# Performance work log

Measured on AMD Instinct MI355X. Metric: run time of the kernel, lower is better.

## Reference

```python
import jax, jax.numpy as jnp
import numpy as np

NUM_HEADS = 16
ROPE_BASE = 10000.0
NEG_INF = float('-inf')


def _rotate_half_interleaved(x):
    # x: [..., d]; interleaved rotation: (-x2, x1) pairs
    x1 = x[..., ::2]
    x2 = x[..., 1::2]
    return jnp.stack((-x2, x1), axis=-1).reshape(x.shape)


def _rope_tables(seq_len, head_dim, dtype):
    inv_freq = 1.0 / (ROPE_BASE ** (jnp.arange(0, head_dim, 2, dtype=jnp.float32) / head_dim))
    pos = jnp.arange(seq_len, dtype=jnp.float32)
    freqs = pos[:, None] * inv_freq[None, :]          # [S, d/2]
    emb = jnp.concatenate((freqs, freqs), axis=-1)    # [S, d]  (HF-style concat, as in source)
    return jnp.cos(emb).astype(dtype), jnp.sin(emb).astype(dtype)


def setup_inputs() -> dict:
    key = jax.random.key(0)
    ks = jax.random.split(key, 4)
    B, S, H = 2, 2048, 2048
    scale = 0.02
    x = jax.random.normal(ks[0], (B, S, H), dtype=jnp.float32)
    qkv_w = jax.random.normal(ks[1], (3 * H, H), dtype=jnp.float32) * scale
    qkv_b = jnp.zeros((3 * H,), dtype=jnp.float32)
    out_w = jax.random.normal(ks[2], (H, H), dtype=jnp.float32) * scale
    out_b = jnp.zeros((H,), dtype=jnp.float32)
    attention_mask = jnp.ones((B, S), dtype=jnp.int32)
    return {"x": x, "attention_mask": attention_mask, "qkv_w": qkv_w,
            "qkv_b": qkv_b, "out_w": out_w, "out_b": out_b}


def reference(x, attention_mask, qkv_w, qkv_b, out_w, out_b):
    B, S, H = x.shape
    nh = NUM_HEADS
    hd = H // nh
    scale = hd ** -0.5

    qkv = x @ qkv_w.T + qkv_b                            # [B,S,3H]
    qkv = qkv.reshape(B, S, 3, nh, hd).transpose(2, 0, 3, 1, 4)  # [3,B,nh,S,hd]
    q, k, v = qkv[0], qkv[1], qkv[2]

    cos, sin = _rope_tables(S, hd, x.dtype)              # [S,hd]
    cos = cos[None, None, :, :]
    sin = sin[None, None, :, :]
    q = q * cos + _rotate_half_interleaved(q) * sin
    k = k * cos + _rotate_half_interleaved(k) * sin

    scores = jnp.einsum('bhqd,bhkd->bhqk', q, k) * scale  # [B,nh,S,S]
    causal = jnp.triu(jnp.ones((S, S), dtype=bool), k=1)
    scores = jnp.where(causal[None, None], NEG_INF, scores)
    key_mask = (attention_mask == 0)[:, None, None, :]    # [B,1,1,S]
    scores = jnp.where(key_mask, NEG_INF, scores)

    weights = jax.nn.softmax(scores, axis=-1)
    attn = jnp.einsum('bhqk,bhkd->bhqd', weights, v)       # [B,nh,S,hd]
    attn = attn.transpose(0, 2, 1, 3).reshape(B, S, H)
    return attn @ out_w.T + out_b
```

## Files before the change

### kernel.cpp

```cpp
#include <hip/hip_runtime.h>

typedef __bf16 bf16;
typedef __bf16 bf16x2 __attribute__((ext_vector_type(2)));
typedef __bf16 bf16x4 __attribute__((ext_vector_type(4)));
typedef __bf16 bf16x8 __attribute__((ext_vector_type(8)));
typedef float f32x4 __attribute__((ext_vector_type(4)));
typedef float f32x16 __attribute__((ext_vector_type(16)));

#define MFMA_BF16(a, b, c) __builtin_amdgcn_mfma_f32_16x16x32_bf16(a, b, c, 0, 0, 0)
#define MFMA32(a, b, c)    __builtin_amdgcn_mfma_f32_32x32x16_bf16(a, b, c, 0, 0, 0)

__device__ __forceinline__ void async16(const void* g, void* l) {
    __builtin_amdgcn_global_load_lds(
        (const __attribute__((address_space(1))) void*)g,
        (__attribute__((address_space(3))) void*)l,
        16, 0, 0);
}

__device__ __forceinline__ unsigned pack2(float a, float b) {
    bf16x2 t; t[0] = (bf16)a; t[1] = (bf16)b;
    return __builtin_bit_cast(unsigned, t);
}

__global__ void cvt8(const float* __restrict__ in, bf16* __restrict__ out, int n) {
    int i = (blockIdx.x * 256 + threadIdx.x) * 8;
    if (i >= n) return;
    float4 a = *(const float4*)(in + i);
    float4 b = *(const float4*)(in + i + 4);
    bf16x8 o;
    o[0] = (bf16)a.x; o[1] = (bf16)a.y; o[2] = (bf16)a.z; o[3] = (bf16)a.w;
    o[4] = (bf16)b.x; o[5] = (bf16)b.y; o[6] = (bf16)b.z; o[7] = (bf16)b.w;
    *(bf16x8*)(out + i) = o;
}

__global__ void tables_k(const int* __restrict__ am, float* __restrict__ cosT,
                         float* __restrict__ sinT, float* __restrict__ mbias) {
    int i = blockIdx.x * 256 + threadIdx.x;
    int s = i >> 7, d = i & 127, fi = d & 63;
    float inv = exp2f(-(float)fi * (13.287712379549449f / 64.0f));
    float ang = (float)s * inv;
    cosT[i] = cosf(ang);
    sinT[i] = sinf(ang);
    if (i < 2 * 2048) mbias[i] = (am[i] == 0) ? -1.4427e30f : 0.0f;
}

template <int EPI>
__global__ void __launch_bounds__(256, 2)
gemm_bt(const bf16* __restrict__ A, const bf16* __restrict__ Bt,
        const float* __restrict__ bias, float* __restrict__ Cf,
        bf16* __restrict__ qb, bf16* __restrict__ kb, bf16* __restrict__ vtb,
        const float* __restrict__ cosT, const float* __restrict__ sinT,
        int M, int N, int K, int bn0) {
    __shared__ __align__(16) bf16 sA[128 * 64];
    __shared__ __align__(16) bf16 sB[128 * 64];
    const int tid  = threadIdx.x;
    const int lane = tid & 63;
    const int quad = lane >> 4, l15 = lane & 15;
    const int wid = tid >> 6, wm = wid >> 1, wn = wid & 1;
    const int bm = blockIdx.x, bn = blockIdx.y + bn0;

    f32x4 acc[4][4];
#pragma unroll
    for (int i = 0; i < 4; i++)
#pragma unroll
        for (int j = 0; j < 4; j++)
#pragma unroll
            for (int c = 0; c < 4; c++) acc[i][j][c] = 0.0f;

    const int r0 = tid >> 3, x0 = tid & 7;
    const int g0 = x0 ^ (r0 & 7);
    const bf16* pa = A  + (size_t)(bm * 128 + r0) * K + g0 * 8;
    const bf16* pb = Bt + (size_t)(bn * 128 + r0) * K + g0 * 8;
    bf16* la = sA + tid * 8;
    bf16* lb = sB + tid * 8;
    const size_t gstep = (size_t)32 * K;

    for (int k0 = 0; k0 < K; k0 += 64) {
#pragma unroll
        for (int i = 0; i < 4; i++) {
            async16(pa + i * gstep, la + i * 2048);
            async16(pb + i * gstep, lb + i * 2048);
        }
        pa += 64; pb += 64;
        __syncthreads();
#pragma unroll
        for (int ks = 0; ks < 2; ks++) {
            bf16x8 af[4], bfr[4];
#pragma unroll
            for (int i = 0; i < 4; i++) {
                int r = wm * 64 + i * 16 + l15;
                int x = (ks * 4 + quad) ^ (r & 7);
                af[i] = *(const bf16x8*)(sA + r * 64 + x * 8);
            }
#pragma unroll
            for (int i = 0; i < 4; i++) {
                int r = wn * 64 + i * 16 + l15;
                int x = (ks * 4 + quad) ^ (r & 7);
                bfr[i] = *(const bf16x8*)(sB + r * 64 + x * 8);
            }
#pragma unroll
            for (int mi = 0; mi < 4; mi++)
#pragma unroll
                for (int ni = 0; ni < 4; ni++)
                    acc[mi][ni] = MFMA_BF16(af[mi], bfr[ni], acc[mi][ni]);
        }
        __syncthreads();
    }

    if (EPI == 0) {
#pragma unroll
        for (int mi = 0; mi < 4; mi++)
#pragma unroll
            for (int ni = 0; ni < 4; ni++) {
                int row0 = bm * 128 + wm * 64 + mi * 16 + quad * 4;
                int col  = bn * 128 + wn * 64 + ni * 16 + l15;
                float bv = bias[col];
#pragma unroll
                for (int r = 0; r < 4; r++)
                    Cf[(size_t)(row0 + r) * N + col] = acc[mi][ni][r] + bv;
            }
    } else {
#pragma unroll
        for (int mi = 0; mi < 4; mi++)
#pragma unroll
            for (int ni = 0; ni < 4; ni++) {
                int col   = bn * 128 + wn * 64 + ni * 16 + l15;
                int which = col >> 11;
                int hcol  = col & 2047;
                int h = hcol >> 7, d = hcol & 127;
                float bv = bias[col];
#pragma unroll
                for (int r = 0; r < 4; r++) {
                    int row = bm * 128 + wm * 64 + mi * 16 + quad * 4 + r;
                    int b = row >> 11, s = row & 2047;
                    float v  = acc[mi][ni][r] + bv;
                    float vp = __shfl_xor(v, 1, 64);
                    float ov = v;
                    if (which < 2) {
                        float c  = cosT[(s << 7) + d];
                        float sn = sinT[(s << 7) + d];
                        ov = v * c + ((d & 1) ? vp : -vp) * sn;
                    }
                    if (which == 0) ov *= 0.12751743f;
                    size_t bh = (size_t)(b * 16 + h);
                    if (which == 0)      qb[(bh * 2048 + s) * 128 + d] = (bf16)ov;
                    else if (which == 1) kb[(bh * 2048 + s) * 128 + d] = (bf16)ov;
                    else                 vtb[(bh * 128 + d) * 2048 + s] = (bf16)ov;
                }
            }
    }
}

__global__ void __launch_bounds__(256, 2)
fattn(const bf16* __restrict__ Q, const bf16* __restrict__ Kg,
      const bf16* __restrict__ Vt, const float* __restrict__ mbias,
      bf16* __restrict__ O) {
    __shared__ __align__(16) bf16 sK[2][64 * 128];
    __shared__ __align__(16) bf16 sV[2][128 * 64];
    const int tid = threadIdx.x, lane = tid & 63, w = tid >> 6;
    const int l31 = lane & 31, half = lane >> 5;
    const int id = (int)blockIdx.x;
    const int round = id >> 8, u = id & 255;
    const int bh = u & 31, j8 = u >> 5;
    const int qt = round ? j8 : 15 - j8;
    const int b = bh >> 4, hh = bh & 15;
    const int myq = qt * 128 + w * 32 + l31;
    const int qmin = qt * 128 + w * 32;

    const bf16* Qb  = Q  + (size_t)bh * 2048 * 128;
    const bf16* Kbh = Kg + (size_t)bh * 2048 * 128;
    const bf16* Vbh = Vt + (size_t)bh * 128 * 2048;
    const float* mbb = mbias + b * 2048;

    const int swk = (l31 & 15) ^ (l31 >> 4);
    const int swv = (l31 & 7) ^ ((l31 >> 3) & 3);

    bf16x8 qf[8];
#pragma unroll
    for (int kq = 0; kq < 8; kq++)
        qf[kq] = *(const bf16x8*)(Qb + (size_t)myq * 128 + kq * 16 + half * 8);

    f32x16 oacc[4];
#pragma unroll
    for (int dt = 0; dt < 4; dt++)
#pragma unroll
        for (int c = 0; c < 16; c++) oacc[dt][c] = 0.0f;
    float m_s = -3e38f, l_s = 0.0f;

    const int rk = tid >> 4, xk = tid & 15, gkb = xk ^ rk;
    const int rv = tid >> 3, xv = tid & 7;
    const int gv = xv ^ (rv & 7) ^ ((rv >> 3) & 3);
    const int nkt = 2 * qt + 2;

#pragma unroll
    for (int i = 0; i < 4; i++) {
        async16(Kbh + (size_t)(rk + i * 16) * 128 + (gkb ^ (i & 1)) * 8,
                &sK[0][(i * 256 + tid) * 8]);
        async16(Vbh + (size_t)(rv + i * 32) * 2048 + gv * 8,
                &sV[0][(i * 256 + tid) * 8]);
    }
    __syncthreads();

    for (int kt = 0; kt < nkt; kt++) {
        const int kb0 = kt * 64;
        const int buf = kt & 1;
        if (kt + 1 < nkt) {
            const int nb0 = kb0 + 64;
#pragma unroll
            for (int i = 0; i < 4; i++) {
                async16(Kbh + (size_t)(nb0 + rk + i * 16) * 128 + (gkb ^ (i & 1)) * 8,
                        &sK[buf ^ 1][(i * 256 + tid) * 8]);
                async16(Vbh + (size_t)(rv + i * 32) * 2048 + nb0 + gv * 8,
                        &sV[buf ^ 1][(i * 256 + tid) * 8]);
            }
        }
        const bf16* sKb = sK[buf];
        const bf16* sVb = sV[buf];

        f32x16 sacc[2];
#pragma unroll
        for (int t = 0; t < 2; t++)
#pragma unroll
            for (int c = 0; c < 16; c++) sacc[t][c] = 0.0f;
#pragma unroll
        for (int kq = 0; kq < 8; kq++) {
#pragma unroll
            for (int t = 0; t < 2; t++) {
                int row = t * 32 + l31;
                int x = (kq * 2 + half) ^ swk;
                bf16x8 kf = *(const bf16x8*)(sKb + row * 128 + x * 8);
                sacc[t] = MFMA32(kf, qf[kq], sacc[t]);
            }
        }

        float mx = -3e38f;
        if (kb0 + 63 < qmin) {
#pragma unroll
            for (int t = 0; t < 2; t++)
#pragma unroll
                for (int g = 0; g < 4; g++) {
                    float4 mb4 = *(const float4*)(mbb + kb0 + t * 32 + 8 * g + 4 * half);
#pragma unroll
                    for (int r2 = 0; r2 < 4; r2++) {
                        float v = sacc[t][g * 4 + r2] + ((const float*)&mb4)[r2];
                        sacc[t][g * 4 + r2] = v;
                        mx = fmaxf(mx, v);
                    }
                }
        } else {
#pragma unroll
            for (int t = 0; t < 2; t++)
#pragma unroll
                for (int g = 0; g < 4; g++) {
                    float4 mb4 = *(const float4*)(mbb + kb0 + t * 32 + 8 * g + 4 * half);
#pragma unroll
                    for (int r2 = 0; r2 < 4; r2++) {
                        int sk = kb0 + t * 32 + 8 * g + 4 * half + r2;
                        float v = sacc[t][g * 4 + r2] + ((const float*)&mb4)[r2];
                        v = (sk > myq) ? -1e30f : v;
                        sacc[t][g * 4 + r2] = v;
                        mx = fmaxf(mx, v);
                    }
                }
        }

        mx = fmaxf(mx, __shfl_xor(mx, 32, 64));
        float mnew  = fmaxf(m_s, mx);
        float alpha = exp2f(m_s - mnew);
        float rs = 0.0f;
#pragma unroll
        for (int t = 0; t < 2; t++)
#pragma unroll
            for (int c = 0; c < 16; c++) {
                float p = exp2f(sacc[t][c] - mnew);
                sacc[t][c] = p;
                rs += p;
            }
        l_s = l_s * alpha + rs;
        m_s = mnew;
#pragma unroll
        for (int dt = 0; dt < 4; dt++) oacc[dt] *= alpha;

#pragma unroll
        for (int t = 0; t < 2; t++) {
            unsigned w8[8];
#pragma unroll
            for (int i = 0; i < 8; i++)
                w8[i] = pack2(sacc[t][2 * i], sacc[t][2 * i + 1]);
#pragma unroll
            for (int s2 = 0; s2 < 2; s2++) {
                const int bse = 4 * s2;
                unsigned a0 = half ? w8[bse]     : w8[bse + 2];
                unsigned a1 = half ? w8[bse + 1] : w8[bse + 3];
                unsigned z0 = (unsigned)__shfl_xor((int)a0, 32, 64);
                unsigned z1 = (unsigned)__shfl_xor((int)a1, 32, 64);
                union { unsigned u[4]; bf16x8 v; } pu;
                pu.u[0] = half ? z0 : w8[bse];
                pu.u[1] = half ? z1 : w8[bse + 1];
                pu.u[2] = half ? w8[bse + 2] : z0;
                pu.u[3] = half ? w8[bse + 3] : z1;
                bf16x8 pf = pu.v;
                const int c = (t * 2 + s2) * 2 + half;
#pragma unroll
                for (int dt = 0; dt < 4; dt++) {
                    int row = dt * 32 + l31;
                    int x = c ^ swv;
                    bf16x8 vf = *(const bf16x8*)(sVb + row * 64 + x * 8);
                    oacc[dt] = MFMA32(vf, pf, oacc[dt]);
                }
            }
        }
        __syncthreads();
    }

    l_s += __shfl_xor(l_s, 32, 64);
    float inv = 1.0f / l_s;
    size_t base = ((size_t)(b * 2048 + myq)) * 2048 + hh * 128;
#pragma unroll
    for (int dt = 0; dt < 4; dt++)
#pragma unroll
        for (int g = 0; g < 4; g++) {
            bf16x4 o4;
#pragma unroll
            for (int r2 = 0; r2 < 4; r2++) o4[r2] = (bf16)(oacc[dt][g * 4 + r2] * inv);
            *(bf16x4*)(O + base + dt * 32 + 8 * g + 4 * half) = o4;
        }
}

extern "C" void kernel_launch(void* const* d_in, const int* in_sizes, int n_in,
                              void* d_out, int out_size, void* d_ws, size_t ws_size,
                              hipStream_t stream) {
    const float* x     = (const float*)d_in[0];
    const int*   am    = (const int*)d_in[1];
    const float* qkvw  = (const float*)d_in[2];
    const float* qkvb  = (const float*)d_in[3];
    const float* outw  = (const float*)d_in[4];
    const float* outb  = (const float*)d_in[5];
    float* out = (float*)d_out;

    char* ws = (char*)d_ws;
    bf16*  xb    = (bf16*)(ws);
    bf16*  wqkv  = (bf16*)(ws + (16ull << 20));
    bf16*  wout  = (bf16*)(ws + (40ull << 20));
    bf16*  qb    = (bf16*)(ws + (48ull << 20));
    bf16*  kb    = (bf16*)(ws + (64ull << 20));
    bf16*  vtb   = (bf16*)(ws + (80ull << 20));
    bf16*  attn  = (bf16*)(ws + (96ull << 20));
    float* cosT  = (float*)(ws + (112ull << 20));
    float* sinT  = (float*)(ws + (113ull << 20));
    float* mbias = (float*)(ws + (114ull << 20));

    cvt8<<<4096, 256, 0, stream>>>(x, xb, 4096 * 2048);
    cvt8<<<6144, 256, 0, stream>>>(qkvw, wqkv, 6144 * 2048);
    cvt8<<<2048, 256, 0, stream>>>(outw, wout, 2048 * 2048);
    tables_k<<<1024, 256, 0, stream>>>(am, cosT, sinT, mbias);

    gemm_bt<1><<<dim3(32, 24), 256, 0, stream>>>(
        xb, wqkv, qkvb, nullptr, qb, kb, vtb, cosT, sinT, 4096, 6144, 2048, 0);
    gemm_bt<1><<<dim3(32, 24), 256, 0, stream>>>(
        xb, wqkv, qkvb, nullptr, qb, kb, vtb, cosT, sinT, 4096, 6144, 2048, 24);

    fattn<<<dim3(512), 256, 0, stream>>>(qb, kb, vtb, mbias, attn);

    gemm_bt<0><<<dim3(32, 16), 256, 0, stream>>>(
        attn, wout, outb, out, nullptr, nullptr, nullptr, nullptr, nullptr,
        4096, 2048, 2048, 0);
}
```

Measured before the change: 409.9 us.

## Balance causal attention work with split-KV pairing and fuse prep kernels

The attention kernel now gives every block exactly 17 key tiles. One role computes the first 17 KV tiles of a long query tile and writes fp32 partials. The other role finishes that long tile's remaining tiles, writes a second partial, then processes a short query tile completely. A new combine kernel merges the two partials with log-sum-exp weights. The four conversion/table kernels are fused into one launch and the QKV GEMM is launched once instead of twice, trading extra partial-buffer traffic and a combine pass for even load across blocks and fewer launches.

```diff
diff --git a/kernel.cpp b/kernel.cpp
--- a/kernel.cpp
+++ b/kernel.cpp
@@ -22,9 +22,9 @@
     return __builtin_bit_cast(unsigned, t);
 }
 
-__global__ void cvt8(const float* __restrict__ in, bf16* __restrict__ out, int n) {
-    int i = (blockIdx.x * 256 + threadIdx.x) * 8;
-    if (i >= n) return;
+__device__ __forceinline__ void cvt8_body(const float* __restrict__ in,
+                                          bf16* __restrict__ out, int blk) {
+    int i = (blk * 256 + (int)threadIdx.x) * 8;
     float4 a = *(const float4*)(in + i);
     float4 b = *(const float4*)(in + i + 4);
     bf16x8 o;
@@ -33,15 +33,24 @@
     *(bf16x8*)(out + i) = o;
 }
 
-__global__ void tables_k(const int* __restrict__ am, float* __restrict__ cosT,
-                         float* __restrict__ sinT, float* __restrict__ mbias) {
-    int i = blockIdx.x * 256 + threadIdx.x;
-    int s = i >> 7, d = i & 127, fi = d & 63;
-    float inv = exp2f(-(float)fi * (13.287712379549449f / 64.0f));
-    float ang = (float)s * inv;
-    cosT[i] = cosf(ang);
-    sinT[i] = sinf(ang);
-    if (i < 2 * 2048) mbias[i] = (am[i] == 0) ? -1.4427e30f : 0.0f;
+__global__ void prep(const float* __restrict__ x, const float* __restrict__ qkvw,
+                     const float* __restrict__ outw, const int* __restrict__ am,
+                     bf16* __restrict__ xb, bf16* __restrict__ wqkv, bf16* __restrict__ wout,
+                     float* __restrict__ cosT, float* __restrict__ sinT,
+                     float* __restrict__ mbias) {
+    int blk = blockIdx.x;
+    if (blk < 4096)        cvt8_body(x,    xb,   blk);
+    else if (blk < 10240)  cvt8_body(qkvw, wqkv, blk - 4096);
+    else if (blk < 12288)  cvt8_body(outw, wout, blk - 10240);
+    else {
+        int i = (blk - 12288) * 256 + threadIdx.x;
+        int s = i >> 7, d = i & 127, fi = d & 63;
+        float inv = exp2f(-(float)fi * (13.287712379549449f / 64.0f));
+        float ang = (float)s * inv;
+        cosT[i] = cosf(ang);
+        sinT[i] = sinf(ang);
+        if (i < 2 * 2048) mbias[i] = (am[i] == 0) ? -1.4427e30f : 0.0f;
+    }
 }
 
 template <int EPI>
@@ -50,14 +59,14 @@
         const float* __restrict__ bias, float* __restrict__ Cf,
         bf16* __restrict__ qb, bf16* __restrict__ kb, bf16* __restrict__ vtb,
         const float* __restrict__ cosT, const float* __restrict__ sinT,
-        int M, int N, int K, int bn0) {
+        int M, int N, int K) {
     __shared__ __align__(16) bf16 sA[128 * 64];
     __shared__ __align__(16) bf16 sB[128 * 64];
     const int tid  = threadIdx.x;
     const int lane = tid & 63;
     const int quad = lane >> 4, l15 = lane & 15;
     const int wid = tid >> 6, wm = wid >> 1, wn = wid & 1;
-    const int bm = blockIdx.x, bn = blockIdx.y + bn0;
+    const int bm = blockIdx.x, bn = blockIdx.y;
 
     f32x4 acc[4][4];
 #pragma unroll
@@ -154,58 +163,93 @@
 __global__ void __launch_bounds__(256, 2)
 fattn(const bf16* __restrict__ Q, const bf16* __restrict__ Kg,
       const bf16* __restrict__ Vt, const float* __restrict__ mbias,
-      bf16* __restrict__ O) {
+      bf16* __restrict__ O, float* __restrict__ Opart, float* __restrict__ mlpart) {
     __shared__ __align__(16) bf16 sK[2][64 * 128];
     __shared__ __align__(16) bf16 sV[2][128 * 64];
     const int tid = threadIdx.x, lane = tid & 63, w = tid >> 6;
     const int l31 = lane & 31, half = lane >> 5;
     const int id = (int)blockIdx.x;
-    const int round = id >> 8, u = id & 255;
-    const int bh = u & 31, j8 = u >> 5;
-    const int qt = round ? j8 : 15 - j8;
-    const int b = bh >> 4, hh = bh & 15;
-    const int myq = qt * 128 + w * 32 + l31;
-    const int qmin = qt * 128 + w * 32;
+    const int bh = id & 31, v = id >> 5;
+    const int p = v >> 1, role = v & 1;
+    const int qa = 15 - p;
+    const int n1 = role ? (15 - 2 * p) : 17;
 
     const bf16* Qb  = Q  + (size_t)bh * 2048 * 128;
     const bf16* Kbh = Kg + (size_t)bh * 2048 * 128;
     const bf16* Vbh = Vt + (size_t)bh * 128 * 2048;
+    const int b = bh >> 4, hh = bh & 15;
     const float* mbb = mbias + b * 2048;
 
     const int swk = (l31 & 15) ^ (l31 >> 4);
     const int swv = (l31 & 7) ^ ((l31 >> 3) & 3);
-
-    bf16x8 qf[8];
-#pragma unroll
-    for (int kq = 0; kq < 8; kq++)
-        qf[kq] = *(const bf16x8*)(Qb + (size_t)myq * 128 + kq * 16 + half * 8);
-
-    f32x16 oacc[4];
-#pragma unroll
-    for (int dt = 0; dt < 4; dt++)
-#pragma unroll
-        for (int c = 0; c < 16; c++) oacc[dt][c] = 0.0f;
-    float m_s = -3e38f, l_s = 0.0f;
-
     const int rk = tid >> 4, xk = tid & 15, gkb = xk ^ rk;
     const int rv = tid >> 3, xv = tid & 7;
     const int gv = xv ^ (rv & 7) ^ ((rv >> 3) & 3);
-    const int nkt = 2 * qt + 2;
-
-#pragma unroll
-    for (int i = 0; i < 4; i++) {
-        async16(Kbh + (size_t)(rk + i * 16) * 128 + (gkb ^ (i & 1)) * 8,
-                &sK[0][(i * 256 + tid) * 8]);
-        async16(Vbh + (size_t)(rv + i * 32) * 2048 + gv * 8,
-                &sV[0][(i * 256 + tid) * 8]);
+
+    auto KT = [&](int t) { return role ? (t < n1 ? 17 + t : t - n1) : t; };
+
+    int qt = qa;
+    int myq  = qt * 128 + w * 32 + l31;
+    int qmin = qt * 128 + w * 32;
+
+    bf16x8 qf[8];
+#pragma unroll
+    for (int kq = 0; kq < 8; kq++)
+        qf[kq] = *(const bf16x8*)(Qb + (size_t)myq * 128 + kq * 16 + half * 8);
+
+    f32x16 oacc[4];
+#pragma unroll
+    for (int dt = 0; dt < 4; dt++)
+#pragma unroll
+        for (int c = 0; c < 16; c++) oacc[dt][c] = 0.0f;
+    float m_s = -3e38f, l_s = 0.0f;
+
+    {
+        int kb0 = KT(0) * 64;
+#pragma unroll
+        for (int i = 0; i < 4; i++) {
+            async16(Kbh + (size_t)(kb0 + rk + i * 16) * 128 + (gkb ^ (i & 1)) * 8,
+                    &sK[0][(i * 256 + tid) * 8]);
+            async16(Vbh + (size_t)(rv + i * 32) * 2048 + kb0 + gv * 8,
+                    &sV[0][(i * 256 + tid) * 8]);
+        }
     }
     __syncthreads();
 
-    for (int kt = 0; kt < nkt; kt++) {
-        const int kb0 = kt * 64;
-        const int buf = kt & 1;
-        if (kt + 1 < nkt) {
-            const int nb0 = kb0 + 64;
+    for (int t = 0; t < 17; t++) {
+        if (role && t == n1) {
+            float lf = l_s + __shfl_xor(l_s, 32, 64);
+            size_t slot = (size_t)(bh * 8 + (qa - 8)) * 2 + 1;
+            float* op = Opart + slot * 16384 + (size_t)(w * 32 + l31) * 128;
+#pragma unroll
+            for (int dt = 0; dt < 4; dt++)
+#pragma unroll
+                for (int g = 0; g < 4; g++) {
+                    float4 o4 = make_float4(oacc[dt][g * 4 + 0], oacc[dt][g * 4 + 1],
+                                            oacc[dt][g * 4 + 2], oacc[dt][g * 4 + 3]);
+                    *(float4*)(op + dt * 32 + 8 * g + 4 * half) = o4;
+                }
+            if (half == 0) {
+                float* mp = mlpart + (slot * 128 + (w * 32 + l31)) * 2;
+                mp[0] = m_s; mp[1] = lf;
+            }
+#pragma unroll
+            for (int dt = 0; dt < 4; dt++)
+#pragma unroll
+                for (int c = 0; c < 16; c++) oacc[dt][c] = 0.0f;
+            m_s = -3e38f; l_s = 0.0f;
+            qt = p;
+            myq  = qt * 128 + w * 32 + l31;
+            qmin = qt * 128 + w * 32;
+#pragma unroll
+            for (int kq = 0; kq < 8; kq++)
+                qf[kq] = *(const bf16x8*)(Qb + (size_t)myq * 128 + kq * 16 + half * 8);
+        }
+
+        const int kb0 = KT(t) * 64;
+        const int buf = t & 1;
+        if (t + 1 < 17) {
+            const int nb0 = KT(t + 1) * 64;
 #pragma unroll
             for (int i = 0; i < 4; i++) {
                 async16(Kbh + (size_t)(nb0 + rk + i * 16) * 128 + (gkb ^ (i & 1)) * 8,
@@ -219,47 +263,47 @@
 
         f32x16 sacc[2];
 #pragma unroll
-        for (int t = 0; t < 2; t++)
-#pragma unroll
-            for (int c = 0; c < 16; c++) sacc[t][c] = 0.0f;
+        for (int tt = 0; tt < 2; tt++)
+#pragma unroll
+            for (int c = 0; c < 16; c++) sacc[tt][c] = 0.0f;
 #pragma unroll
         for (int kq = 0; kq < 8; kq++) {
 #pragma unroll
-            for (int t = 0; t < 2; t++) {
-                int row = t * 32 + l31;
+            for (int tt = 0; tt < 2; tt++) {
+                int row = tt * 32 + l31;
                 int x = (kq * 2 + half) ^ swk;
                 bf16x8 kf = *(const bf16x8*)(sKb + row * 128 + x * 8);
-                sacc[t] = MFMA32(kf, qf[kq], sacc[t]);
+                sacc[tt] = MFMA32(kf, qf[kq], sacc[tt]);
             }
         }
 
         float mx = -3e38f;
         if (kb0 + 63 < qmin) {
 #pragma unroll
-            for (int t = 0; t < 2; t++)
+            for (int tt = 0; tt < 2; tt++)
 #pragma unroll
                 for (int g = 0; g < 4; g++) {
-                    float4 mb4 = *(const float4*)(mbb + kb0 + t * 32 + 8 * g + 4 * half);
+                    float4 mb4 = *(const float4*)(mbb + kb0 + tt * 32 + 8 * g + 4 * half);
 #pragma unroll
                     for (int r2 = 0; r2 < 4; r2++) {
-                        float v = sacc[t][g * 4 + r2] + ((const float*)&mb4)[r2];
-                        sacc[t][g * 4 + r2] = v;
-                        mx = fmaxf(mx, v);
+                        float vv = sacc[tt][g * 4 + r2] + ((const float*)&mb4)[r2];
+                        sacc[tt][g * 4 + r2] = vv;
+                        mx = fmaxf(mx, vv);
                     }
                 }
         } else {
 #pragma unroll
-            for (int t = 0; t < 2; t++)
+            for (int tt = 0; tt < 2; tt++)
 #pragma unroll
                 for (int g = 0; g < 4; g++) {
-                    float4 mb4 = *(const float4*)(mbb + kb0 + t * 32 + 8 * g + 4 * half);
+                    float4 mb4 = *(const float4*)(mbb + kb0 + tt * 32 + 8 * g + 4 * half);
 #pragma unroll
                     for (int r2 = 0; r2 < 4; r2++) {
-                        int sk = kb0 + t * 32 + 8 * g + 4 * half + r2;
-                        float v = sacc[t][g * 4 + r2] + ((const float*)&mb4)[r2];
-                        v = (sk > myq) ? -1e30f : v;
-                        sacc[t][g * 4 + r2] = v;
-                        mx = fmaxf(mx, v);
+                        int sk = kb0 + tt * 32 + 8 * g + 4 * half + r2;
+                        float vv = sacc[tt][g * 4 + r2] + ((const float*)&mb4)[r2];
+                        vv = (sk > myq) ? -1e30f : vv;
+                        sacc[tt][g * 4 + r2] = vv;
+                        mx = fmaxf(mx, vv);
                     }
                 }
         }
@@ -269,12 +313,12 @@
         float alpha = exp2f(m_s - mnew);
         float rs = 0.0f;
 #pragma unroll
-        for (int t = 0; t < 2; t++)
+        for (int tt = 0; tt < 2; tt++)
 #pragma unroll
             for (int c = 0; c < 16; c++) {
-                float p = exp2f(sacc[t][c] - mnew);
-                sacc[t][c] = p;
-                rs += p;
+                float pe = exp2f(sacc[tt][c] - mnew);
+                sacc[tt][c] = pe;
+                rs += pe;
             }
         l_s = l_s * alpha + rs;
         m_s = mnew;
@@ -282,11 +326,11 @@
         for (int dt = 0; dt < 4; dt++) oacc[dt] *= alpha;
 
 #pragma unroll
-        for (int t = 0; t < 2; t++) {
+        for (int tt = 0; tt < 2; tt++) {
             unsigned w8[8];
 #pragma unroll
             for (int i = 0; i < 8; i++)
-                w8[i] = pack2(sacc[t][2 * i], sacc[t][2 * i + 1]);
+                w8[i] = pack2(sacc[tt][2 * i], sacc[tt][2 * i + 1]);
 #pragma unroll
             for (int s2 = 0; s2 < 2; s2++) {
                 const int bse = 4 * s2;
@@ -294,13 +338,13 @@
                 unsigned a1 = half ? w8[bse + 1] : w8[bse + 3];
                 unsigned z0 = (unsigned)__shfl_xor((int)a0, 32, 64);
                 unsigned z1 = (unsigned)__shfl_xor((int)a1, 32, 64);
-                union { unsigned u[4]; bf16x8 v; } pu;
+                union { unsigned u[4]; bf16x8 vv; } pu;
                 pu.u[0] = half ? z0 : w8[bse];
                 pu.u[1] = half ? z1 : w8[bse + 1];
                 pu.u[2] = half ? w8[bse + 2] : z0;
                 pu.u[3] = half ? w8[bse + 3] : z1;
-                bf16x8 pf = pu.v;
-                const int c = (t * 2 + s2) * 2 + half;
+                bf16x8 pf = pu.vv;
+                const int c = (tt * 2 + s2) * 2 + half;
 #pragma unroll
                 for (int dt = 0; dt < 4; dt++) {
                     int row = dt * 32 + l31;
@@ -313,18 +357,60 @@
         __syncthreads();
     }
 
-    l_s += __shfl_xor(l_s, 32, 64);
-    float inv = 1.0f / l_s;
-    size_t base = ((size_t)(b * 2048 + myq)) * 2048 + hh * 128;
-#pragma unroll
-    for (int dt = 0; dt < 4; dt++)
-#pragma unroll
-        for (int g = 0; g < 4; g++) {
-            bf16x4 o4;
-#pragma unroll
-            for (int r2 = 0; r2 < 4; r2++) o4[r2] = (bf16)(oacc[dt][g * 4 + r2] * inv);
-            *(bf16x4*)(O + base + dt * 32 + 8 * g + 4 * half) = o4;
-        }
+    float lf = l_s + __shfl_xor(l_s, 32, 64);
+    if (role == 0) {
+        size_t slot = (size_t)(bh * 8 + (qa - 8)) * 2 + 0;
+        float* op = Opart + slot * 16384 + (size_t)(w * 32 + l31) * 128;
+#pragma unroll
+        for (int dt = 0; dt < 4; dt++)
+#pragma unroll
+            for (int g = 0; g < 4; g++) {
+                float4 o4 = make_float4(oacc[dt][g * 4 + 0], oacc[dt][g * 4 + 1],
+                                        oacc[dt][g * 4 + 2], oacc[dt][g * 4 + 3]);
+                *(float4*)(op + dt * 32 + 8 * g + 4 * half) = o4;
+            }
+        if (half == 0) {
+            float* mp = mlpart + (slot * 128 + (w * 32 + l31)) * 2;
+            mp[0] = m_s; mp[1] = lf;
+        }
+    } else {
+        float inv = 1.0f / lf;
+        size_t base = ((size_t)(b * 2048 + myq)) * 2048 + hh * 128;
+#pragma unroll
+        for (int dt = 0; dt < 4; dt++)
+#pragma unroll
+            for (int g = 0; g < 4; g++) {
+                bf16x4 o4;
+#pragma unroll
+                for (int r2 = 0; r2 < 4; r2++) o4[r2] = (bf16)(oacc[dt][g * 4 + r2] * inv);
+                *(bf16x4*)(O + base + dt * 32 + 8 * g + 4 * half) = o4;
+            }
+    }
+}
+
+__global__ void combine(const float* __restrict__ Opart, const float* __restrict__ mlpart,
+                        bf16* __restrict__ attn) {
+    int i = blockIdx.x * 256 + threadIdx.x;
+    int dq = (i & 31) * 4;
+    int row = i >> 5;
+    int qloc = row & 127, ba = row >> 7;
+    int ai = ba & 7, bh = ba >> 3;
+    const float* mlA = mlpart + ((size_t)(ba * 2 + 0) * 128 + qloc) * 2;
+    const float* mlB = mlpart + ((size_t)(ba * 2 + 1) * 128 + qloc) * 2;
+    float mA = mlA[0], lA = mlA[1], mB = mlB[0], lB = mlB[1];
+    float m = fmaxf(mA, mB);
+    float wA = exp2f(mA - m), wB = exp2f(mB - m);
+    float inv = 1.0f / (wA * lA + wB * lB);
+    float4 oA = *(const float4*)(Opart + (size_t)(ba * 2 + 0) * 16384 + qloc * 128 + dq);
+    float4 oB = *(const float4*)(Opart + (size_t)(ba * 2 + 1) * 16384 + qloc * 128 + dq);
+    int q = (8 + ai) * 128 + qloc;
+    int b = bh >> 4, hh = bh & 15;
+    bf16x4 o4;
+    o4[0] = (bf16)((wA * oA.x + wB * oB.x) * inv);
+    o4[1] = (bf16)((wA * oA.y + wB * oB.y) * inv);
+    o4[2] = (bf16)((wA * oA.z + wB * oB.z) * inv);
+    o4[3] = (bf16)((wA * oA.w + wB * oB.w) * inv);
+    *(bf16x4*)(attn + ((size_t)(b * 2048 + q)) * 2048 + hh * 128 + dq) = o4;
 }
 
 extern "C" void kernel_launch(void* const* d_in, const int* in_sizes, int n_in,
@@ -349,20 +435,19 @@
     float* cosT  = (float*)(ws + (112ull << 20));
     float* sinT  = (float*)(ws + (113ull << 20));
     float* mbias = (float*)(ws + (114ull << 20));
-
-    cvt8<<<4096, 256, 0, stream>>>(x, xb, 4096 * 2048);
-    cvt8<<<6144, 256, 0, stream>>>(qkvw, wqkv, 6144 * 2048);
-    cvt8<<<2048, 256, 0, stream>>>(outw, wout, 2048 * 2048);
-    tables_k<<<1024, 256, 0, stream>>>(am, cosT, sinT, mbias);
-
-    gemm_bt<1><<<dim3(32, 24), 256, 0, stream>>>(
-        xb, wqkv, qkvb, nullptr, qb, kb, vtb, cosT, sinT, 4096, 6144, 2048, 0);
-    gemm_bt<1><<<dim3(32, 24), 256, 0, stream>>>(
-        xb, wqkv, qkvb, nullptr, qb, kb, vtb, cosT, sinT, 4096, 6144, 2048, 24);
-
-    fattn<<<dim3(512), 256, 0, stream>>>(qb, kb, vtb, mbias, attn);
+    float* Opart  = (float*)(ws);
+    float* mlpart = (float*)(ws + (32ull << 20));
+
+    prep<<<13312, 256, 0, stream>>>(x, qkvw, outw, am, xb, wqkv, wout, cosT, sinT, mbias);
+
+    gemm_bt<1><<<dim3(32, 48), 256, 0, stream>>>(
+        xb, wqkv, qkvb, nullptr, qb, kb, vtb, cosT, sinT, 4096, 6144, 2048);
+
+    fattn<<<dim3(512), 256, 0, stream>>>(qb, kb, vtb, mbias, attn, Opart, mlpart);
+
+    combine<<<4096, 256, 0, stream>>>(Opart, mlpart, attn);
 
     gemm_bt<0><<<dim3(32, 16), 256, 0, stream>>>(
         attn, wout, outb, out, nullptr, nullptr, nullptr, nullptr, nullptr,
-        4096, 2048, 2048, 0);
-}
+        4096, 2048, 2048);
+}
```

Measured after the change: 385.6 us. 1.06x faster.
